# Kernel tuning notes

Measured on AMD Instinct MI355X. Metric: run time of the kernel, lower is better.

Reference implementation:

```python
import jax, jax.numpy as jnp
import numpy as np

KLD_SCALE = 10.0
COMMITMENT_COST = 0.25


def setup_inputs() -> dict:
    key = jax.random.key(0)
    k1, k2 = jax.random.split(key)
    B, N, D, K = 8192, 32, 64, 1024
    z = jax.random.normal(k1, (B, N, D), dtype=jnp.float32)
    embed_w = jax.random.normal(k2, (K, N * D), dtype=jnp.float32)
    return {"z": z, "embed_w": embed_w}


def reference(z, embed_w):
    B, N, D = z.shape
    zf = z.reshape(B, N * D)  # b (n d)
    # squared L2 distance to each codebook vector via GEMM expansion
    dist = (jnp.sum(zf * zf, axis=1, keepdims=True)
            - 2.0 * zf @ embed_w.T
            + jnp.sum(embed_w * embed_w, axis=1)[None, :])  # [B, K]
    ind = jnp.argmin(dist, axis=1)  # [B]
    z_q = embed_w[ind]  # [B, N*D] gather
    latent_loss = (COMMITMENT_COST * jnp.mean((jax.lax.stop_gradient(z_q) - zf) ** 2)
                   + jnp.mean((z_q - jax.lax.stop_gradient(zf)) ** 2))
    latent_loss = latent_loss * KLD_SCALE
    z_q = zf + jax.lax.stop_gradient(z_q - zf)  # straight-through
    return z_q, latent_loss
```

## Files before the change

### kernel.cpp

```cpp
#include <hip/hip_runtime.h>

#define NB 8192
#define NK 1024
#define ND 2048
#define DELTA 4.0f

typedef __bf16 bf16x8 __attribute__((ext_vector_type(8)));
typedef float f32x4 __attribute__((ext_vector_type(4)));

static __device__ __forceinline__ unsigned short f2bf(float f) {
    unsigned u = __float_as_uint(f);
    unsigned r = (u + 0x7fff + ((u >> 16) & 1)) >> 16;
    return (unsigned short)r;
}

static __device__ __forceinline__ void async16(const void* g, void* l) {
    __builtin_amdgcn_global_load_lds(
        (const __attribute__((address_space(1))) void*)g,
        (__attribute__((address_space(3))) void*)l, 16, 0, 0);
}

static __device__ __forceinline__ unsigned skey(float s) {
    unsigned u = __float_as_uint(s);
    return (s >= 0.f) ? (u | 0x80000000u) : ~u;
}

__global__ __launch_bounds__(256)
void conv_z_kernel(const float* __restrict__ z, unsigned short* __restrict__ zh,
                   float* __restrict__ znorm) {
    const int w = threadIdx.x >> 6, l = threadIdx.x & 63;
    const int b = blockIdx.x * 4 + w;
    const float4* row = (const float4*)(z + (size_t)b * ND);
    ushort4* orow = (ushort4*)(zh + (size_t)b * ND);
    float s = 0.f;
#pragma unroll
    for (int i = 0; i < 8; ++i) {
        float4 v = row[l + 64 * i];
        s += v.x * v.x + v.y * v.y + v.z * v.z + v.w * v.w;
        ushort4 h;
        h.x = f2bf(v.x); h.y = f2bf(v.y); h.z = f2bf(v.z); h.w = f2bf(v.w);
        orow[l + 64 * i] = h;
    }
#pragma unroll
    for (int m = 32; m; m >>= 1) s += __shfl_xor(s, m, 64);
    if (l == 0) znorm[b] = s;
}

__global__ void conv_e_kernel(const float* __restrict__ e, unsigned short* __restrict__ eh,
                              float* __restrict__ enorm) {
    const int k = blockIdx.x;
    const int l = threadIdx.x;
    const float4* row = (const float4*)(e + (size_t)k * ND);
    ushort4* orow = (ushort4*)(eh + (size_t)k * ND);
    float s = 0.f;
#pragma unroll
    for (int i = 0; i < 8; ++i) {
        float4 v = row[l + 64 * i];
        s += v.x * v.x + v.y * v.y + v.z * v.z + v.w * v.w;
        ushort4 h;
        h.x = f2bf(v.x); h.y = f2bf(v.y); h.z = f2bf(v.z); h.w = f2bf(v.w);
        orow[l + 64 * i] = h;
    }
#pragma unroll
    for (int m = 32; m; m >>= 1) s += __shfl_xor(s, m, 64);
    if (l == 0) enorm[k] = s;
}

__global__ __launch_bounds__(256)
void coarse_gemm_kernel(const unsigned short* __restrict__ zh,
                        const unsigned short* __restrict__ eh,
                        const float* __restrict__ enorm,
                        float* __restrict__ pmin, ulonglong2* __restrict__ pmask) {
    __shared__ __align__(16) unsigned short As[128 * 64];
    __shared__ __align__(16) unsigned short Bs[128 * 64];
    __shared__ float rmin[128][2];
    __shared__ unsigned long long rmask[128][2];

    const int t = threadIdx.x;
    const int w = t >> 6, l = t & 63;
    const int wr = w & 1, wc = w >> 1;
    const int rowBase = blockIdx.x * 128;
    const int colBase = blockIdx.y * 128;

    f32x4 acc[4][4];
#pragma unroll
    for (int m = 0; m < 4; ++m)
#pragma unroll
        for (int n = 0; n < 4; ++n) acc[m][n] = (f32x4)(0.0f);

    const int r0  = t >> 3;
    const int csw = (t & 7) ^ (r0 & 7);
    const size_t zsrc = (size_t)(rowBase + r0) * ND + csw * 8;
    const size_t esrc = (size_t)(colBase + r0) * ND + csw * 8;

    for (int k0 = 0; k0 < ND; k0 += 64) {
#pragma unroll
        for (int i = 0; i < 4; ++i) {
            async16(zh + zsrc + (size_t)i * 32 * ND + k0, &As[i * 2048 + w * 512]);
            async16(eh + esrc + (size_t)i * 32 * ND + k0, &Bs[i * 2048 + w * 512]);
        }
        __syncthreads();
#pragma unroll
        for (int kk = 0; kk < 2; ++kk) {
            bf16x8 af[4], bfr[4];
#pragma unroll
            for (int m = 0; m < 4; ++m) {
                int r = wr * 64 + m * 16 + (l & 15);
                int ch = ((l >> 4) + kk * 4) ^ (l & 7);
                af[m] = *(const bf16x8*)&As[r * 64 + ch * 8];
            }
#pragma unroll
            for (int n = 0; n < 4; ++n) {
                int r = wc * 64 + n * 16 + (l & 15);
                int ch = ((l >> 4) + kk * 4) ^ (l & 7);
                bfr[n] = *(const bf16x8*)&Bs[r * 64 + ch * 8];
            }
#pragma unroll
            for (int m = 0; m < 4; ++m)
#pragma unroll
                for (int n = 0; n < 4; ++n)
                    acc[m][n] = __builtin_amdgcn_mfma_f32_16x16x32_bf16(af[m], bfr[n], acc[m][n], 0, 0, 0);
        }
        __syncthreads();
    }

    float en[4];
#pragma unroll
    for (int n = 0; n < 4; ++n)
        en[n] = enorm[colBase + wc * 64 + n * 16 + (l & 15)];
    const int g = l >> 4;

#pragma unroll
    for (int m = 0; m < 4; ++m) {
#pragma unroll
        for (int j = 0; j < 4; ++j) {
            float mn = 3.0e38f;
#pragma unroll
            for (int n = 0; n < 4; ++n)
                mn = fminf(mn, en[n] - 2.0f * acc[m][n][j]);
#pragma unroll
            for (int d = 1; d < 16; d <<= 1) mn = fminf(mn, __shfl_xor(mn, d, 64));
            if ((l & 15) == 0) rmin[wr * 64 + m * 16 + g * 4 + j][wc] = mn;
        }
    }
    __syncthreads();

#pragma unroll
    for (int m = 0; m < 4; ++m) {
#pragma unroll
        for (int j = 0; j < 4; ++j) {
            int rl = wr * 64 + m * 16 + g * 4 + j;
            float thr = fminf(rmin[rl][0], rmin[rl][1]) + DELTA;
            unsigned long long seg = 0;
#pragma unroll
            for (int n = 0; n < 4; ++n) {
                unsigned long long bal = __ballot((en[n] - 2.0f * acc[m][n][j]) <= thr);
                seg |= ((bal >> (16 * g)) & 0xFFFFull) << (n * 16);
            }
            if ((l & 15) == 0) rmask[rl][wc] = seg;
        }
    }
    __syncthreads();
    if (t < 128) {
        size_t idx = (size_t)(rowBase + t) * 8 + blockIdx.y;
        pmin[idx] = fminf(rmin[t][0], rmin[t][1]);
        ulonglong2 mk; mk.x = rmask[t][0]; mk.y = rmask[t][1];
        pmask[idx] = mk;
    }
}

__global__ __launch_bounds__(256)
void resolve2_kernel(const float* __restrict__ pmin, const ulonglong2* __restrict__ pmask,
                     const float* __restrict__ z, const float* __restrict__ e,
                     const float* __restrict__ enorm, unsigned long long* __restrict__ best) {
    const int w = threadIdx.x >> 6, l = threadIdx.x & 63;
    const int b = blockIdx.x * 4 + w;

    float v = pmin[(size_t)b * 8 + (l & 7)];
#pragma unroll
    for (int d = 1; d < 8; d <<= 1) v = fminf(v, __shfl_xor(v, d, 64));
    const float thr = v + DELTA;

    unsigned long long mlo = 0, mhi = 0;
    int cnt = 0, kc = -1;
    if (l < 8) {
        float pc = pmin[(size_t)b * 8 + l];
        if (pc <= thr) {
            ulonglong2 mk = pmask[(size_t)b * 8 + l];
            mlo = mk.x; mhi = mk.y;
            cnt = __popcll(mlo) + __popcll(mhi);
            if (cnt) kc = l * 128 + (mlo ? (__ffsll((long long)mlo) - 1)
                                         : 64 + (__ffsll((long long)mhi) - 1));
        }
    }
    int tot = cnt;
#pragma unroll
    for (int d = 1; d < 8; d <<= 1) {
        tot += __shfl_xor(tot, d, 64);
        kc = max(kc, __shfl_xor(kc, d, 64));
    }
    tot = __shfl(tot, 0, 64);
    kc  = __shfl(kc, 0, 64);

    if (tot == 1) {
        if (l == 0) best[b] = ((unsigned long long)skey(v) << 32) | (unsigned)kc;
        return;
    }

    float bestv = 3.0e38f; int bestk = 0x7fffffff;
    const float4* z4 = (const float4*)(z + (size_t)b * ND);
    for (int c = 0; c < 8; ++c) {
        unsigned long long lo = __shfl(mlo, c, 64);
        unsigned long long hi = __shfl(mhi, c, 64);
        while (lo | hi) {
            int k;
            if (lo) { int bit = __ffsll((long long)lo) - 1; lo &= lo - 1; k = c * 128 + bit; }
            else    { int bit = __ffsll((long long)hi) - 1; hi &= hi - 1; k = c * 128 + 64 + bit; }
            const float4* e4 = (const float4*)(e + (size_t)k * ND);
            float dot = 0.f;
#pragma unroll
            for (int q = 0; q < 8; ++q) {
                float4 a = z4[l + 64 * q], bb = e4[l + 64 * q];
                dot += a.x * bb.x + a.y * bb.y + a.z * bb.z + a.w * bb.w;
            }
#pragma unroll
            for (int d2 = 32; d2; d2 >>= 1) dot += __shfl_xor(dot, d2, 64);
            float s = enorm[k] - 2.0f * dot;
            if (s < bestv) { bestv = s; bestk = k; }
        }
    }
    if (l == 0) best[b] = ((unsigned long long)skey(bestv) << 32) | (unsigned)bestk;
}

__global__ __launch_bounds__(256)
void loss_kernel(const unsigned long long* __restrict__ best,
                 const float* __restrict__ znorm, float* __restrict__ loss) {
    const int b = blockIdx.x * 256 + threadIdx.x;
    unsigned long long p = best[b];
    unsigned key = (unsigned)(p >> 32);
    unsigned ub = (key & 0x80000000u) ? (key ^ 0x80000000u) : ~key;
    float s = __uint_as_float(ub);
    float c = znorm[b] + s;
#pragma unroll
    for (int m = 32; m; m >>= 1) c += __shfl_xor(c, m, 64);
    __shared__ float red[4];
    int lane = threadIdx.x & 63, w = threadIdx.x >> 6;
    if (lane == 0) red[w] = c;
    __syncthreads();
    if (threadIdx.x == 0) {
        float t = (red[0] + red[1]) + (red[2] + red[3]);
        atomicAdd(loss, t * (12.5f / 16777216.0f));
    }
}

__global__ __launch_bounds__(256)
void gather_kernel(const float* __restrict__ e, const unsigned long long* __restrict__ best,
                   float* __restrict__ out) {
    const int NT4 = NB * ND / 4;
    for (int f = blockIdx.x * blockDim.x + threadIdx.x; f < NT4;
         f += gridDim.x * blockDim.x) {
        int b  = f >> 9;
        int k4 = f & 511;
        int k = (int)(best[b] & 1023ull);
        ((float4*)out)[f] = *(const float4*)(e + (size_t)k * ND + (size_t)k4 * 4);
    }
}

#define BK 16
#define LDS_STRIDE 20

__global__ void enorm_kernel(const float* __restrict__ e, float* __restrict__ enorm) {
    const int k = blockIdx.x;
    const int lane = threadIdx.x;
    const float4* row = (const float4*)(e + (size_t)k * ND);
    float s = 0.f;
#pragma unroll
    for (int i = 0; i < 8; ++i) {
        float4 v = row[lane + 64 * i];
        s += v.x * v.x + v.y * v.y + v.z * v.z + v.w * v.w;
    }
#pragma unroll
    for (int m = 32; m; m >>= 1) s += __shfl_xor(s, m, 64);
    if (lane == 0) enorm[k] = s;
}

__global__ __launch_bounds__(256, 2)
void argmin_kernel(const float* __restrict__ z, const float* __restrict__ e,
                   const float* __restrict__ enorm,
                   float* __restrict__ pminv, int* __restrict__ pmini) {
    __shared__ float zs[128 * LDS_STRIDE];
    __shared__ float es[128 * LDS_STRIDE];
    const int t  = threadIdx.x;
    const int tx = t & 31;
    const int ty = t >> 5;
    const int rowBase = blockIdx.x * 128;
    const int colBase = blockIdx.y * 128;

    float acc[16][4];
#pragma unroll
    for (int i = 0; i < 16; ++i)
#pragma unroll
        for (int j = 0; j < 4; ++j) acc[i][j] = 0.f;

    const int srow = t >> 2;
    const int sc4  = t & 3;

    for (int k0 = 0; k0 < ND; k0 += BK) {
#pragma unroll
        for (int q = 0; q < 2; ++q) {
            int r = srow + 64 * q;
            float4 vz = *(const float4*)(z + (size_t)(rowBase + r) * ND + k0 + sc4 * 4);
            *(float4*)(zs + r * LDS_STRIDE + sc4 * 4) = vz;
            float4 ve = *(const float4*)(e + (size_t)(colBase + r) * ND + k0 + sc4 * 4);
            *(float4*)(es + r * LDS_STRIDE + sc4 * 4) = ve;
        }
        __syncthreads();
#pragma unroll
        for (int g = 0; g < BK / 4; ++g) {
            float4 ef[4];
#pragma unroll
            for (int j = 0; j < 4; ++j)
                ef[j] = *(const float4*)(es + (tx + 32 * j) * LDS_STRIDE + g * 4);
#pragma unroll
            for (int i = 0; i < 16; ++i) {
                float4 zf = *(const float4*)(zs + (ty + 8 * i) * LDS_STRIDE + g * 4);
#pragma unroll
                for (int j = 0; j < 4; ++j) {
                    acc[i][j] += zf.x * ef[j].x;
                    acc[i][j] += zf.y * ef[j].y;
                    acc[i][j] += zf.z * ef[j].z;
                    acc[i][j] += zf.w * ef[j].w;
                }
            }
        }
        __syncthreads();
    }
#pragma unroll
    for (int i = 0; i < 16; ++i) {
        float bv = 3.0e38f; int bi = 0x7fffffff;
#pragma unroll
        for (int j = 0; j < 4; ++j) {
            int cg = colBase + tx + 32 * j;
            float s = enorm[cg] - 2.0f * acc[i][j];
            if (s < bv) { bv = s; bi = cg; }
        }
#pragma unroll
        for (int m = 16; m; m >>= 1) {
            float ov = __shfl_xor(bv, m, 64);
            int   oi = __shfl_xor(bi, m, 64);
            if (ov < bv || (ov == bv && oi < bi)) { bv = ov; bi = oi; }
        }
        if (tx == 0) {
            int r = rowBase + ty + 8 * i;
            pminv[(size_t)r * 8 + blockIdx.y] = bv;
            pmini[(size_t)r * 8 + blockIdx.y] = bi;
        }
    }
}

__global__ void final_argmin_kernel(const float* __restrict__ pminv,
                                    const int* __restrict__ pmini,
                                    int* __restrict__ ind) {
    int b = blockIdx.x * 256 + threadIdx.x;
    if (b >= NB) return;
    float bv = pminv[(size_t)b * 8];
    int   bi = pmini[(size_t)b * 8];
#pragma unroll
    for (int c = 1; c < 8; ++c) {
        float v  = pminv[(size_t)b * 8 + c];
        int   i2 = pmini[(size_t)b * 8 + c];
        if (v < bv || (v == bv && i2 < bi)) { bv = v; bi = i2; }
    }
    ind[b] = bi;
}

__global__ __launch_bounds__(256)
void gather_loss_kernel(const float* __restrict__ z, const float* __restrict__ e,
                        const int* __restrict__ ind, float* __restrict__ out,
                        float* __restrict__ loss) {
    const int NT4 = NB * ND / 4;
    float accm = 0.f;
    for (int f = blockIdx.x * blockDim.x + threadIdx.x; f < NT4;
         f += gridDim.x * blockDim.x) {
        int b  = f >> 9;
        int k4 = f & 511;
        const float4 q  = *(const float4*)(e + (size_t)ind[b] * ND + (size_t)k4 * 4);
        const float4 zz = *(const float4*)(z + (size_t)f * 4);
        *(float4*)(out + (size_t)f * 4) = q;
        float dx = q.x - zz.x, dy = q.y - zz.y, dz = q.z - zz.z, dw = q.w - zz.w;
        accm += dx * dx + dy * dy + dz * dz + dw * dw;
    }
#pragma unroll
    for (int m = 32; m; m >>= 1) accm += __shfl_xor(accm, m, 64);
    __shared__ float red[4];
    int lane = threadIdx.x & 63, w = threadIdx.x >> 6;
    if (lane == 0) red[w] = accm;
    __syncthreads();
    if (threadIdx.x == 0) {
        float s = (red[0] + red[1]) + (red[2] + red[3]);
        atomicAdd(loss, s * (12.5f / 16777216.0f));
    }
}

extern "C" void kernel_launch(void* const* d_in, const int* in_sizes, int n_in,
                              void* d_out, int out_size, void* d_ws, size_t ws_size,
                              hipStream_t stream) {
    const float* z = (const float*)d_in[0];
    const float* e = (const float*)d_in[1];
    float* out  = (float*)d_out;
    float* loss = out + (size_t)NB * ND;
    char* W = (char*)d_ws;

    const size_t OFF_ZH    = 0;
    const size_t OFF_EH    = 33554432;
    const size_t OFF_PMIN  = 37748736;
    const size_t OFF_PMASK = 38010880;
    const size_t OFF_EN    = 39059456;
    const size_t OFF_ZN    = 39063552;
    const size_t OFF_BEST  = 39096320;
    const size_t NEED_FAST = 39161856 + 4096;

    hipMemsetAsync(loss, 0, sizeof(float), stream);

    if (ws_size >= NEED_FAST) {
        unsigned short* zh = (unsigned short*)(W + OFF_ZH);
        unsigned short* eh = (unsigned short*)(W + OFF_EH);
        float* pmin        = (float*)(W + OFF_PMIN);
        ulonglong2* pmask  = (ulonglong2*)(W + OFF_PMASK);
        float* enorm       = (float*)(W + OFF_EN);
        float* znorm       = (float*)(W + OFF_ZN);
        unsigned long long* best = (unsigned long long*)(W + OFF_BEST);

        hipLaunchKernelGGL(conv_z_kernel, dim3(NB / 4), dim3(256), 0, stream, z, zh, znorm);
        hipLaunchKernelGGL(conv_e_kernel, dim3(NK), dim3(64), 0, stream, e, eh, enorm);
        hipLaunchKernelGGL(coarse_gemm_kernel, dim3(NB / 128, NK / 128), dim3(256), 0, stream,
                           zh, eh, enorm, pmin, pmask);
        hipLaunchKernelGGL(resolve2_kernel, dim3(NB / 4), dim3(256), 0, stream,
                           pmin, pmask, z, e, enorm, best);
        hipLaunchKernelGGL(loss_kernel, dim3(NB / 256), dim3(256), 0, stream,
                           best, znorm, loss);
        hipLaunchKernelGGL(gather_kernel, dim3(2048), dim3(256), 0, stream, e, best, out);
    } else {
        float* enorm = (float*)W;
        float* pminv = (float*)(W + 4096);
        int*   pmini = (int*)(W + 4096 + 262144);
        int*   ind   = (int*)(W + 4096 + 524288);

        hipLaunchKernelGGL(enorm_kernel, dim3(NK), dim3(64), 0, stream, e, enorm);
        hipLaunchKernelGGL(argmin_kernel, dim3(NB / 128, NK / 128), dim3(256), 0, stream,
                           z, e, enorm, pminv, pmini);
        hipLaunchKernelGGL(final_argmin_kernel, dim3(NB / 256), dim3(256), 0, stream,
                           pminv, pmini, ind);
        hipLaunchKernelGGL(gather_loss_kernel, dim3(2048), dim3(256), 0, stream,
                           z, e, ind, out, loss);
    }
}
```

Measured before the change: 90.80 us.

## Fuse z bf16 conversion and norm into coarse GEMM A-tile loading

Removes the separate conv_z pass: the coarse GEMM now reads fp32 z straight from global memory, converts it to bf16 in registers, writes it into the swizzled LDS tile and prefetches the next k-slice during compute. The first column of blocks also accumulates the total squared norm of z into a single atomic scalar, so the loss kernel becomes a one-block reduction that writes the loss directly. This avoids writing and re-reading a 32MB bf16 copy of z. In exchange, z is read as fp32 (twice the bytes) by each of the 8 column blocks, and the A-tile load becomes a synchronous register path instead of async global-to-LDS.

Result: slower. 122.6 us (+35.0%).

```diff
diff --git a/kernel.cpp b/kernel.cpp
--- a/kernel.cpp
+++ b/kernel.cpp
@@ -23,27 +23,6 @@
 static __device__ __forceinline__ unsigned skey(float s) {
     unsigned u = __float_as_uint(s);
     return (s >= 0.f) ? (u | 0x80000000u) : ~u;
-}
-
-__global__ __launch_bounds__(256)
-void conv_z_kernel(const float* __restrict__ z, unsigned short* __restrict__ zh,
-                   float* __restrict__ znorm) {
-    const int w = threadIdx.x >> 6, l = threadIdx.x & 63;
-    const int b = blockIdx.x * 4 + w;
-    const float4* row = (const float4*)(z + (size_t)b * ND);
-    ushort4* orow = (ushort4*)(zh + (size_t)b * ND);
-    float s = 0.f;
-#pragma unroll
-    for (int i = 0; i < 8; ++i) {
-        float4 v = row[l + 64 * i];
-        s += v.x * v.x + v.y * v.y + v.z * v.z + v.w * v.w;
-        ushort4 h;
-        h.x = f2bf(v.x); h.y = f2bf(v.y); h.z = f2bf(v.z); h.w = f2bf(v.w);
-        orow[l + 64 * i] = h;
-    }
-#pragma unroll
-    for (int m = 32; m; m >>= 1) s += __shfl_xor(s, m, 64);
-    if (l == 0) znorm[b] = s;
 }
 
 __global__ void conv_e_kernel(const float* __restrict__ e, unsigned short* __restrict__ eh,
@@ -67,14 +46,16 @@
 }
 
 __global__ __launch_bounds__(256)
-void coarse_gemm_kernel(const unsigned short* __restrict__ zh,
+void coarse_gemm_kernel(const float* __restrict__ z,
                         const unsigned short* __restrict__ eh,
                         const float* __restrict__ enorm,
-                        float* __restrict__ pmin, ulonglong2* __restrict__ pmask) {
+                        float* __restrict__ pmin, ulonglong2* __restrict__ pmask,
+                        float* __restrict__ znsum) {
     __shared__ __align__(16) unsigned short As[128 * 64];
     __shared__ __align__(16) unsigned short Bs[128 * 64];
     __shared__ float rmin[128][2];
     __shared__ unsigned long long rmask[128][2];
+    __shared__ float zred[4];
 
     const int t = threadIdx.x;
     const int w = t >> 6, l = t & 63;
@@ -88,18 +69,45 @@
 #pragma unroll
         for (int n = 0; n < 4; ++n) acc[m][n] = (f32x4)(0.0f);
 
+    const int rA = t >> 1;
+    const int cb = (t & 1) * 4;
+    const float4* z4 = (const float4*)(z + (size_t)(rowBase + rA) * ND + cb * 8);
+
     const int r0  = t >> 3;
     const int csw = (t & 7) ^ (r0 & 7);
-    const size_t zsrc = (size_t)(rowBase + r0) * ND + csw * 8;
     const size_t esrc = (size_t)(colBase + r0) * ND + csw * 8;
 
+    const bool accz = (blockIdx.y == 0);
+    float zn = 0.f;
+
+    float4 ar[8];
+#pragma unroll
+    for (int j = 0; j < 8; ++j) ar[j] = z4[j];
+
     for (int k0 = 0; k0 < ND; k0 += 64) {
 #pragma unroll
-        for (int i = 0; i < 4; ++i) {
-            async16(zh + zsrc + (size_t)i * 32 * ND + k0, &As[i * 2048 + w * 512]);
+        for (int j2 = 0; j2 < 4; ++j2) {
+            float4 a = ar[2 * j2], b2 = ar[2 * j2 + 1];
+            union { bf16x8 v; __bf16 e[8]; } u;
+            u.e[0] = (__bf16)a.x;  u.e[1] = (__bf16)a.y;
+            u.e[2] = (__bf16)a.z;  u.e[3] = (__bf16)a.w;
+            u.e[4] = (__bf16)b2.x; u.e[5] = (__bf16)b2.y;
+            u.e[6] = (__bf16)b2.z; u.e[7] = (__bf16)b2.w;
+            *(bf16x8*)&As[rA * 64 + ((cb + j2) ^ (rA & 7)) * 8] = u.v;
+            if (accz)
+                zn += a.x * a.x + a.y * a.y + a.z * a.z + a.w * a.w
+                    + b2.x * b2.x + b2.y * b2.y + b2.z * b2.z + b2.w * b2.w;
+        }
+#pragma unroll
+        for (int i = 0; i < 4; ++i)
             async16(eh + esrc + (size_t)i * 32 * ND + k0, &Bs[i * 2048 + w * 512]);
-        }
         __syncthreads();
+
+        if (k0 + 64 < ND) {
+#pragma unroll
+            for (int j = 0; j < 8; ++j) ar[j] = z4[((k0 + 64) >> 2) + j];
+        }
+
 #pragma unroll
         for (int kk = 0; kk < 2; ++kk) {
             bf16x8 af[4], bfr[4];
@@ -166,6 +174,14 @@
         pmin[idx] = fminf(rmin[t][0], rmin[t][1]);
         ulonglong2 mk; mk.x = rmask[t][0]; mk.y = rmask[t][1];
         pmask[idx] = mk;
+    }
+
+    if (accz) {
+#pragma unroll
+        for (int m = 32; m; m >>= 1) zn += __shfl_xor(zn, m, 64);
+        if (l == 0) zred[w] = zn;
+        __syncthreads();
+        if (t == 0) atomicAdd(znsum, (zred[0] + zred[1]) + (zred[2] + zred[3]));
     }
 }
 
@@ -234,22 +250,22 @@
 
 __global__ __launch_bounds__(256)
 void loss_kernel(const unsigned long long* __restrict__ best,
-                 const float* __restrict__ znorm, float* __restrict__ loss) {
-    const int b = blockIdx.x * 256 + threadIdx.x;
-    unsigned long long p = best[b];
-    unsigned key = (unsigned)(p >> 32);
-    unsigned ub = (key & 0x80000000u) ? (key ^ 0x80000000u) : ~key;
-    float s = __uint_as_float(ub);
-    float c = znorm[b] + s;
-#pragma unroll
-    for (int m = 32; m; m >>= 1) c += __shfl_xor(c, m, 64);
+                 const float* __restrict__ znsum, float* __restrict__ loss) {
+    float s = 0.f;
+    for (int b = threadIdx.x; b < NB; b += 256) {
+        unsigned key = (unsigned)(best[b] >> 32);
+        unsigned ub = (key & 0x80000000u) ? (key ^ 0x80000000u) : ~key;
+        s += __uint_as_float(ub);
+    }
+#pragma unroll
+    for (int m = 32; m; m >>= 1) s += __shfl_xor(s, m, 64);
     __shared__ float red[4];
     int lane = threadIdx.x & 63, w = threadIdx.x >> 6;
-    if (lane == 0) red[w] = c;
+    if (lane == 0) red[w] = s;
     __syncthreads();
     if (threadIdx.x == 0) {
-        float t = (red[0] + red[1]) + (red[2] + red[3]);
-        atomicAdd(loss, t * (12.5f / 16777216.0f));
+        float t = (red[0] + red[1]) + (red[2] + red[3]) + *znsum;
+        loss[0] = t * (12.5f / 16777216.0f);
     }
 }
 
@@ -411,34 +427,30 @@
     float* loss = out + (size_t)NB * ND;
     char* W = (char*)d_ws;
 
-    const size_t OFF_ZH    = 0;
-    const size_t OFF_EH    = 33554432;
-    const size_t OFF_PMIN  = 37748736;
-    const size_t OFF_PMASK = 38010880;
-    const size_t OFF_EN    = 39059456;
-    const size_t OFF_ZN    = 39063552;
-    const size_t OFF_BEST  = 39096320;
-    const size_t NEED_FAST = 39161856 + 4096;
-
-    hipMemsetAsync(loss, 0, sizeof(float), stream);
+    const size_t OFF_EH    = 0;
+    const size_t OFF_PMIN  = 4194304;
+    const size_t OFF_PMASK = 4456448;
+    const size_t OFF_EN    = 5505024;
+    const size_t OFF_BEST  = 5509120;
+    const size_t OFF_ZNS   = 5574656;
+    const size_t NEED_FAST = 5578752 + 4096;
 
     if (ws_size >= NEED_FAST) {
-        unsigned short* zh = (unsigned short*)(W + OFF_ZH);
         unsigned short* eh = (unsigned short*)(W + OFF_EH);
         float* pmin        = (float*)(W + OFF_PMIN);
         ulonglong2* pmask  = (ulonglong2*)(W + OFF_PMASK);
         float* enorm       = (float*)(W + OFF_EN);
-        float* znorm       = (float*)(W + OFF_ZN);
         unsigned long long* best = (unsigned long long*)(W + OFF_BEST);
-
-        hipLaunchKernelGGL(conv_z_kernel, dim3(NB / 4), dim3(256), 0, stream, z, zh, znorm);
+        float* znsum       = (float*)(W + OFF_ZNS);
+
+        hipMemsetAsync(znsum, 0, sizeof(float), stream);
         hipLaunchKernelGGL(conv_e_kernel, dim3(NK), dim3(64), 0, stream, e, eh, enorm);
         hipLaunchKernelGGL(coarse_gemm_kernel, dim3(NB / 128, NK / 128), dim3(256), 0, stream,
-                           zh, eh, enorm, pmin, pmask);
+                           z, eh, enorm, pmin, pmask, znsum);
         hipLaunchKernelGGL(resolve2_kernel, dim3(NB / 4), dim3(256), 0, stream,
                            pmin, pmask, z, e, enorm, best);
-        hipLaunchKernelGGL(loss_kernel, dim3(NB / 256), dim3(256), 0, stream,
-                           best, znorm, loss);
+        hipLaunchKernelGGL(loss_kernel, dim3(1), dim3(256), 0, stream,
+                           best, znsum, loss);
         hipLaunchKernelGGL(gather_kernel, dim3(2048), dim3(256), 0, stream, e, best, out);
     } else {
         float* enorm = (float*)W;
@@ -446,6 +458,7 @@
         int*   pmini = (int*)(W + 4096 + 262144);
         int*   ind   = (int*)(W + 4096 + 524288);
 
+        hipMemsetAsync(loss, 0, sizeof(float), stream);
         hipLaunchKernelGGL(enorm_kernel, dim3(NK), dim3(64), 0, stream, e, enorm);
         hipLaunchKernelGGL(argmin_kernel, dim3(NB / 128, NK / 128), dim3(256), 0, stream,
                            z, e, enorm, pminv, pmini);
```

## Fuse conversion kernels and merge resolve, loss and gather into one tail kernel

Applied to the files above, without the earlier changes.

The separate z and codebook bf16 conversion kernels become one prep kernel with a combined grid. The argmin resolve, loss reduction and output gather are merged into a single tail kernel, so each row's winning codebook entry is copied right after it is chosen and the loss atomic is issued per block. This removes three launches and the round trip through the best-index buffer. In exchange, the loss now takes one atomic per 4-row block instead of one per 256 rows, and the gather is no longer a grid-stride loop.

After: 98.47 us. +8.4%, slower.

```diff
diff --git a/kernel.cpp b/kernel.cpp
--- a/kernel.cpp
+++ b/kernel.cpp
@@ -25,13 +25,11 @@
     return (s >= 0.f) ? (u | 0x80000000u) : ~u;
 }
 
-__global__ __launch_bounds__(256)
-void conv_z_kernel(const float* __restrict__ z, unsigned short* __restrict__ zh,
-                   float* __restrict__ znorm) {
-    const int w = threadIdx.x >> 6, l = threadIdx.x & 63;
-    const int b = blockIdx.x * 4 + w;
-    const float4* row = (const float4*)(z + (size_t)b * ND);
-    ushort4* orow = (ushort4*)(zh + (size_t)b * ND);
+static __device__ __forceinline__ void conv_row(const float* __restrict__ src,
+                                                unsigned short* __restrict__ dst,
+                                                float* __restrict__ nrm, int l) {
+    const float4* row = (const float4*)src;
+    ushort4* orow = (ushort4*)dst;
     float s = 0.f;
 #pragma unroll
     for (int i = 0; i < 8; ++i) {
@@ -43,27 +41,21 @@
     }
 #pragma unroll
     for (int m = 32; m; m >>= 1) s += __shfl_xor(s, m, 64);
-    if (l == 0) znorm[b] = s;
-}
-
-__global__ void conv_e_kernel(const float* __restrict__ e, unsigned short* __restrict__ eh,
-                              float* __restrict__ enorm) {
-    const int k = blockIdx.x;
-    const int l = threadIdx.x;
-    const float4* row = (const float4*)(e + (size_t)k * ND);
-    ushort4* orow = (ushort4*)(eh + (size_t)k * ND);
-    float s = 0.f;
-#pragma unroll
-    for (int i = 0; i < 8; ++i) {
-        float4 v = row[l + 64 * i];
-        s += v.x * v.x + v.y * v.y + v.z * v.z + v.w * v.w;
-        ushort4 h;
-        h.x = f2bf(v.x); h.y = f2bf(v.y); h.z = f2bf(v.z); h.w = f2bf(v.w);
-        orow[l + 64 * i] = h;
-    }
-#pragma unroll
-    for (int m = 32; m; m >>= 1) s += __shfl_xor(s, m, 64);
-    if (l == 0) enorm[k] = s;
+    if (l == 0) *nrm = s;
+}
+
+__global__ __launch_bounds__(256)
+void prep_kernel(const float* __restrict__ z, const float* __restrict__ e,
+                 unsigned short* __restrict__ zh, unsigned short* __restrict__ eh,
+                 float* __restrict__ znorm, float* __restrict__ enorm) {
+    const int w = threadIdx.x >> 6, l = threadIdx.x & 63;
+    if (blockIdx.x < NB / 4) {
+        const int b = blockIdx.x * 4 + w;
+        conv_row(z + (size_t)b * ND, zh + (size_t)b * ND, znorm + b, l);
+    } else {
+        const int k = (blockIdx.x - NB / 4) * 4 + w;
+        conv_row(e + (size_t)k * ND, eh + (size_t)k * ND, enorm + k, l);
+    }
 }
 
 __global__ __launch_bounds__(256)
@@ -170,9 +162,11 @@
 }
 
 __global__ __launch_bounds__(256)
-void resolve2_kernel(const float* __restrict__ pmin, const ulonglong2* __restrict__ pmask,
-                     const float* __restrict__ z, const float* __restrict__ e,
-                     const float* __restrict__ enorm, unsigned long long* __restrict__ best) {
+void tail_kernel(const float* __restrict__ pmin, const ulonglong2* __restrict__ pmask,
+                 const float* __restrict__ z, const float* __restrict__ e,
+                 const float* __restrict__ enorm, const float* __restrict__ znorm,
+                 float* __restrict__ out, float* __restrict__ loss) {
+    __shared__ float red[4];
     const int w = threadIdx.x >> 6, l = threadIdx.x & 63;
     const int b = blockIdx.x * 4 + w;
 
@@ -202,67 +196,47 @@
     tot = __shfl(tot, 0, 64);
     kc  = __shfl(kc, 0, 64);
 
+    int bestk;
+    float srow;
     if (tot == 1) {
-        if (l == 0) best[b] = ((unsigned long long)skey(v) << 32) | (unsigned)kc;
-        return;
-    }
-
-    float bestv = 3.0e38f; int bestk = 0x7fffffff;
-    const float4* z4 = (const float4*)(z + (size_t)b * ND);
-    for (int c = 0; c < 8; ++c) {
-        unsigned long long lo = __shfl(mlo, c, 64);
-        unsigned long long hi = __shfl(mhi, c, 64);
-        while (lo | hi) {
-            int k;
-            if (lo) { int bit = __ffsll((long long)lo) - 1; lo &= lo - 1; k = c * 128 + bit; }
-            else    { int bit = __ffsll((long long)hi) - 1; hi &= hi - 1; k = c * 128 + 64 + bit; }
-            const float4* e4 = (const float4*)(e + (size_t)k * ND);
-            float dot = 0.f;
-#pragma unroll
-            for (int q = 0; q < 8; ++q) {
-                float4 a = z4[l + 64 * q], bb = e4[l + 64 * q];
-                dot += a.x * bb.x + a.y * bb.y + a.z * bb.z + a.w * bb.w;
+        bestk = kc;
+        srow  = v;
+    } else {
+        float bestv = 3.0e38f; bestk = 0x7fffffff;
+        const float4* z4 = (const float4*)(z + (size_t)b * ND);
+        for (int c = 0; c < 8; ++c) {
+            unsigned long long lo = __shfl(mlo, c, 64);
+            unsigned long long hi = __shfl(mhi, c, 64);
+            while (lo | hi) {
+                int k;
+                if (lo) { int bit = __ffsll((long long)lo) - 1; lo &= lo - 1; k = c * 128 + bit; }
+                else    { int bit = __ffsll((long long)hi) - 1; hi &= hi - 1; k = c * 128 + 64 + bit; }
+                const float4* e4 = (const float4*)(e + (size_t)k * ND);
+                float dot = 0.f;
+#pragma unroll
+                for (int q = 0; q < 8; ++q) {
+                    float4 a = z4[l + 64 * q], bb = e4[l + 64 * q];
+                    dot += a.x * bb.x + a.y * bb.y + a.z * bb.z + a.w * bb.w;
+                }
+#pragma unroll
+                for (int d2 = 32; d2; d2 >>= 1) dot += __shfl_xor(dot, d2, 64);
+                float s = enorm[k] - 2.0f * dot;
+                if (s < bestv) { bestv = s; bestk = k; }
             }
-#pragma unroll
-            for (int d2 = 32; d2; d2 >>= 1) dot += __shfl_xor(dot, d2, 64);
-            float s = enorm[k] - 2.0f * dot;
-            if (s < bestv) { bestv = s; bestk = k; }
-        }
-    }
-    if (l == 0) best[b] = ((unsigned long long)skey(bestv) << 32) | (unsigned)bestk;
-}
-
-__global__ __launch_bounds__(256)
-void loss_kernel(const unsigned long long* __restrict__ best,
-                 const float* __restrict__ znorm, float* __restrict__ loss) {
-    const int b = blockIdx.x * 256 + threadIdx.x;
-    unsigned long long p = best[b];
-    unsigned key = (unsigned)(p >> 32);
-    unsigned ub = (key & 0x80000000u) ? (key ^ 0x80000000u) : ~key;
-    float s = __uint_as_float(ub);
-    float c = znorm[b] + s;
-#pragma unroll
-    for (int m = 32; m; m >>= 1) c += __shfl_xor(c, m, 64);
-    __shared__ float red[4];
-    int lane = threadIdx.x & 63, w = threadIdx.x >> 6;
-    if (lane == 0) red[w] = c;
+        }
+        srow = bestv;
+    }
+
+    const float4* q4 = (const float4*)(e + (size_t)bestk * ND);
+    float4* o4 = (float4*)(out + (size_t)b * ND);
+#pragma unroll
+    for (int i = 0; i < 8; ++i) o4[l + 64 * i] = q4[l + 64 * i];
+
+    if (l == 0) red[w] = znorm[b] + srow;
     __syncthreads();
     if (threadIdx.x == 0) {
-        float t = (red[0] + red[1]) + (red[2] + red[3]);
-        atomicAdd(loss, t * (12.5f / 16777216.0f));
-    }
-}
-
-__global__ __launch_bounds__(256)
-void gather_kernel(const float* __restrict__ e, const unsigned long long* __restrict__ best,
-                   float* __restrict__ out) {
-    const int NT4 = NB * ND / 4;
-    for (int f = blockIdx.x * blockDim.x + threadIdx.x; f < NT4;
-         f += gridDim.x * blockDim.x) {
-        int b  = f >> 9;
-        int k4 = f & 511;
-        int k = (int)(best[b] & 1023ull);
-        ((float4*)out)[f] = *(const float4*)(e + (size_t)k * ND + (size_t)k4 * 4);
+        float s = (red[0] + red[1]) + (red[2] + red[3]);
+        atomicAdd(loss, s * (12.5f / 16777216.0f));
     }
 }
 
@@ -417,8 +391,7 @@
     const size_t OFF_PMASK = 38010880;
     const size_t OFF_EN    = 39059456;
     const size_t OFF_ZN    = 39063552;
-    const size_t OFF_BEST  = 39096320;
-    const size_t NEED_FAST = 39161856 + 4096;
+    const size_t NEED_FAST = 39096320 + 4096;
 
     hipMemsetAsync(loss, 0, sizeof(float), stream);
 
@@ -429,17 +402,13 @@
         ulonglong2* pmask  = (ulonglong2*)(W + OFF_PMASK);
         float* enorm       = (float*)(W + OFF_EN);
         float* znorm       = (float*)(W + OFF_ZN);
-        unsigned long long* best = (unsigned long long*)(W + OFF_BEST);
-
-        hipLaunchKernelGGL(conv_z_kernel, dim3(NB / 4), dim3(256), 0, stream, z, zh, znorm);
-        hipLaunchKernelGGL(conv_e_kernel, dim3(NK), dim3(64), 0, stream, e, eh, enorm);
+
+        hipLaunchKernelGGL(prep_kernel, dim3(NB / 4 + NK / 4), dim3(256), 0, stream,
+                           z, e, zh, eh, znorm, enorm);
         hipLaunchKernelGGL(coarse_gemm_kernel, dim3(NB / 128, NK / 128), dim3(256), 0, stream,
                            zh, eh, enorm, pmin, pmask);
-        hipLaunchKernelGGL(resolve2_kernel, dim3(NB / 4), dim3(256), 0, stream,
-                           pmin, pmask, z, e, enorm, best);
-        hipLaunchKernelGGL(loss_kernel, dim3(NB / 256), dim3(256), 0, stream,
-                           best, znorm, loss);
-        hipLaunchKernelGGL(gather_kernel, dim3(2048), dim3(256), 0, stream, e, best, out);
+        hipLaunchKernelGGL(tail_kernel, dim3(NB / 4), dim3(256), 0, stream,
+                           pmin, pmask, z, e, enorm, znorm, out, loss);
     } else {
         float* enorm = (float*)W;
         float* pminv = (float*)(W + 4096);
```
